# Kernel tuning notes

Measured on AMD Instinct MI355X. Metric: run time of the kernel, lower is better.

The kernel has to match this reference:

```python
import jax, jax.numpy as jnp
import numpy as np

TAU = 1.0
LOSS_WEIGHT = 1.0
N = 4_000_000


def setup_inputs() -> dict:
    key = jax.random.key(0)
    k1, k2 = jax.random.split(key)

    def make_boxes(k):
        u = jax.random.uniform(k, (N, 5), dtype=jnp.float32)
        xy = u[:, :2] * 1024.0                 # centers in a 1024px image
        wh = u[:, 2:4] * 100.0 + 4.0           # box sizes in [4, 104)
        r = (u[:, 4:5] - 0.5) * jnp.pi         # angle in [-pi/2, pi/2)
        return jnp.concatenate([xy, wh, r], axis=-1)

    return {"pred": make_boxes(k1), "target": make_boxes(k2)}


def xy_wh_r_2_xy_sigma(xywhr):
    """(N,5) rbox -> (mu (N,2), sigma (N,2,2)) via R @ (S/2)^2 @ R^T closed form."""
    xy = xywhr[..., :2]
    wh = jnp.clip(xywhr[..., 2:4], 1e-7, 1e7)
    r = xywhr[..., 4]
    c, s = jnp.cos(r), jnp.sin(r)
    a = (0.5 * wh[..., 0]) ** 2  # (w/2)^2
    b = (0.5 * wh[..., 1]) ** 2  # (h/2)^2
    s00 = a * c * c + b * s * s
    s11 = a * s * s + b * c * c
    s01 = (a - b) * s * c
    sigma = jnp.stack(
        [jnp.stack([s00, s01], -1), jnp.stack([s01, s11], -1)], -2
    )  # (N,2,2)
    return xy, sigma


def _det2(m):
    return m[..., 0, 0] * m[..., 1, 1] - m[..., 0, 1] * m[..., 1, 0]


def _inv2(m):
    det = _det2(m)
    adj = jnp.stack(
        [jnp.stack([m[..., 1, 1], -m[..., 0, 1]], -1),
         jnp.stack([-m[..., 1, 0], m[..., 0, 0]], -1)], -2)
    return adj / det[..., None, None]


def kld_loss(mu_p, sigma_p, mu_t, sigma_t, tau):
    delta = mu_p - mu_t                                # (N,2)
    sigma_t_inv = _inv2(sigma_t)                       # (N,2,2)
    # delta^T Sigma_t^{-1} delta
    term1 = jnp.einsum('ni,nij,nj->n', delta, sigma_t_inv, delta)
    # tr(Sigma_t^{-1} Sigma_p) + log(det Sigma_t / det Sigma_p)
    tr = jnp.einsum('nij,nji->n', sigma_t_inv, sigma_p)
    term2 = tr + jnp.log(_det2(sigma_t) / _det2(sigma_p))
    dis = term1 + term2 - 2.0
    kl_dis = jnp.maximum(dis, 1e-6)
    # fun == 'log1p'
    loss = 1.0 - 1.0 / (tau + jnp.log1p(kl_dis))
    return loss[:, None]                               # (N,1) like torch version


def reference(pred, target):
    mu_p, sigma_p = xy_wh_r_2_xy_sigma(pred)
    mu_t, sigma_t = xy_wh_r_2_xy_sigma(target)
    return kld_loss(mu_p, sigma_p, mu_t, sigma_t, TAU) * LOSS_WEIGHT
```

## Files before the change

kernel.cpp:

```cpp
#include <hip/hip_runtime.h>
#include <math.h>

#define TAU_CONST 1.0f
#define BLOCK 256

#define INV_PI 0.31830988618f
#define LN2    0.69314718056f

__device__ __forceinline__ float fast_rcp(float x) { return __builtin_amdgcn_rcpf(x); }
__device__ __forceinline__ float fast_log2(float x) { return __builtin_amdgcn_logf(x); }

__device__ __forceinline__ float kld_row(const float* p, const float* t) {
    float pw = fminf(fmaxf(p[2], 1e-7f), 1e7f), ph = fminf(fmaxf(p[3], 1e-7f), 1e7f);
    float tw = fminf(fmaxf(t[2], 1e-7f), 1e7f), th = fminf(fmaxf(t[3], 1e-7f), 1e7f);
    float ap = 0.25f * pw * pw, bp = 0.25f * ph * ph;
    float at = 0.25f * tw * tw, bt = 0.25f * th * th;

    float revp = p[4] * INV_PI;
    float revt = t[4] * INV_PI;
    float s2p = __builtin_amdgcn_sinf(revp), c2p = __builtin_amdgcn_cosf(revp);
    float s2t = __builtin_amdgcn_sinf(revt), c2t = __builtin_amdgcn_cosf(revt);

    float hp = 0.5f * (ap + bp), qp = 0.5f * (ap - bp);
    float ht = 0.5f * (at + bt), qt = 0.5f * (at - bt);
    float p00 = hp + qp * c2p, p11 = hp - qp * c2p, p01 = qp * s2p;
    float t00 = ht + qt * c2t, t11 = ht - qt * c2t, t01 = qt * s2t;

    float dp = ap * bp;
    float dt = at * bt;
    float inv_dt = fast_rcp(dt);

    float dx = p[0] - t[0], dy = p[1] - t[1];
    float term1 = (dx * dx * t11 - 2.0f * dx * dy * t01 + dy * dy * t00) * inv_dt;
    float tr    = (t11 * p00 + t00 * p11 - 2.0f * t01 * p01) * inv_dt;
    float logterm = LN2 * fast_log2(dt * fast_rcp(dp));

    float dis = term1 + tr + logterm - 2.0f;
    float kl  = fmaxf(dis, 1e-6f);
    float denom = TAU_CONST + LN2 * fast_log2(1.0f + kl);
    return 1.0f - fast_rcp(denom);
}

__global__ void __launch_bounds__(BLOCK) gdloss_hw_kernel(const float4* __restrict__ pred4,
                                                          const float4* __restrict__ targ4,
                                                          float4* __restrict__ out4, int n4) {
    int tid = blockIdx.x * blockDim.x + threadIdx.x;
    if (tid >= n4) return;
    float4 pv[5], tv[5];
    const long b = 5L * tid;
#pragma unroll
    for (int k = 0; k < 5; ++k) {
        pv[k] = pred4[b + k];
        tv[k] = targ4[b + k];
    }
    const float* P = (const float*)pv;
    const float* T = (const float*)tv;
    float4 o;
    o.x = kld_row(P + 0,  T + 0);
    o.y = kld_row(P + 5,  T + 5);
    o.z = kld_row(P + 10, T + 10);
    o.w = kld_row(P + 15, T + 15);
    out4[tid] = o;
}

__global__ void gdloss_tail_kernel(const float* __restrict__ pred,
                                   const float* __restrict__ target,
                                   float* __restrict__ out, int start, int n) {
    int i = start + blockIdx.x * blockDim.x + threadIdx.x;
    if (i >= n) return;
    float p[5], t[5];
#pragma unroll
    for (int k = 0; k < 5; ++k) { p[k] = pred[5 * i + k]; t[k] = target[5 * i + k]; }
    out[i] = kld_row(p, t);
}

extern "C" void kernel_launch(void* const* d_in, const int* in_sizes, int n_in,
                              void* d_out, int out_size, void* d_ws, size_t ws_size,
                              hipStream_t stream) {
    const float* pred   = (const float*)d_in[0];
    const float* target = (const float*)d_in[1];
    float* out = (float*)d_out;
    const int n = in_sizes[0] / 5;
    const int n4 = n / 4;
    if (n4 > 0) {
        int blocks = (n4 + BLOCK - 1) / BLOCK;
        gdloss_hw_kernel<<<blocks, BLOCK, 0, stream>>>((const float4*)pred,
                                                       (const float4*)target,
                                                       (float4*)out, n4);
    }
    if (n - n4 * 4 > 0) {
        gdloss_tail_kernel<<<1, 64, 0, stream>>>(pred, target, out, n4 * 4, n);
    }
}
```

Baseline: 178.4 us.

## Stage input tiles into LDS via async global_load_lds with double buffering

Replaces the one-row-group-per-thread kernel with a persistent grid-stride kernel. Each wavefront copies 256-row tiles of pred and target straight into LDS using global_load_lds and double-buffers them, so the next tile's loads overlap the current tile's math. The aim is to hide memory latency and make the input reads fully coalesced. In exchange it adds LDS traffic, a hand-written vmcnt wait, and a capped grid of 1024 blocks of 128 threads, which may lower occupancy.

```diff
diff --git a/kernel.cpp b/kernel.cpp
--- a/kernel.cpp
+++ b/kernel.cpp
@@ -2,10 +2,15 @@
 #include <math.h>
 
 #define TAU_CONST 1.0f
-#define BLOCK 256
+#define BLOCK 128
+#define WPB (BLOCK / 64)
+#define NBLOCKS 1024
+#define ROWS_PER_TILE 256
 
 #define INV_PI 0.31830988618f
 #define LN2    0.69314718056f
+
+typedef float vfloat4 __attribute__((ext_vector_type(4)));
 
 __device__ __forceinline__ float fast_rcp(float x) { return __builtin_amdgcn_rcpf(x); }
 __device__ __forceinline__ float fast_log2(float x) { return __builtin_amdgcn_logf(x); }
@@ -15,52 +20,72 @@
     float tw = fminf(fmaxf(t[2], 1e-7f), 1e7f), th = fminf(fmaxf(t[3], 1e-7f), 1e7f);
     float ap = 0.25f * pw * pw, bp = 0.25f * ph * ph;
     float at = 0.25f * tw * tw, bt = 0.25f * th * th;
-
-    float revp = p[4] * INV_PI;
-    float revt = t[4] * INV_PI;
-    float s2p = __builtin_amdgcn_sinf(revp), c2p = __builtin_amdgcn_cosf(revp);
-    float s2t = __builtin_amdgcn_sinf(revt), c2t = __builtin_amdgcn_cosf(revt);
-
+    float s2p = __builtin_amdgcn_sinf(p[4] * INV_PI), c2p = __builtin_amdgcn_cosf(p[4] * INV_PI);
+    float s2t = __builtin_amdgcn_sinf(t[4] * INV_PI), c2t = __builtin_amdgcn_cosf(t[4] * INV_PI);
     float hp = 0.5f * (ap + bp), qp = 0.5f * (ap - bp);
     float ht = 0.5f * (at + bt), qt = 0.5f * (at - bt);
     float p00 = hp + qp * c2p, p11 = hp - qp * c2p, p01 = qp * s2p;
     float t00 = ht + qt * c2t, t11 = ht - qt * c2t, t01 = qt * s2t;
-
-    float dp = ap * bp;
-    float dt = at * bt;
+    float dp = ap * bp, dt = at * bt;
     float inv_dt = fast_rcp(dt);
-
     float dx = p[0] - t[0], dy = p[1] - t[1];
     float term1 = (dx * dx * t11 - 2.0f * dx * dy * t01 + dy * dy * t00) * inv_dt;
     float tr    = (t11 * p00 + t00 * p11 - 2.0f * t01 * p01) * inv_dt;
     float logterm = LN2 * fast_log2(dt * fast_rcp(dp));
-
     float dis = term1 + tr + logterm - 2.0f;
     float kl  = fmaxf(dis, 1e-6f);
-    float denom = TAU_CONST + LN2 * fast_log2(1.0f + kl);
-    return 1.0f - fast_rcp(denom);
+    return 1.0f - fast_rcp(TAU_CONST + LN2 * fast_log2(1.0f + kl));
 }
 
-__global__ void __launch_bounds__(BLOCK) gdloss_hw_kernel(const float4* __restrict__ pred4,
-                                                          const float4* __restrict__ targ4,
-                                                          float4* __restrict__ out4, int n4) {
-    int tid = blockIdx.x * blockDim.x + threadIdx.x;
-    if (tid >= n4) return;
-    float4 pv[5], tv[5];
-    const long b = 5L * tid;
+__device__ __forceinline__ void stage_tile(const char* predB, const char* targB,
+                                           int t, float* buf, int lane) {
+    const char* gp = predB + (size_t)t * 5120 + (size_t)lane * 16;
+    const char* gt = targB + (size_t)t * 5120 + (size_t)lane * 16;
+    float* lp = buf;
+    float* lt = buf + 1280;
 #pragma unroll
-    for (int k = 0; k < 5; ++k) {
-        pv[k] = pred4[b + k];
-        tv[k] = targ4[b + k];
+    for (int i = 0; i < 5; ++i) {
+        __builtin_amdgcn_global_load_lds((const __attribute__((address_space(1))) void*)(gp + i * 1024),
+                                         (__attribute__((address_space(3))) void*)(lp + i * 256), 16, 0, 0);
+        __builtin_amdgcn_global_load_lds((const __attribute__((address_space(1))) void*)(gt + i * 1024),
+                                         (__attribute__((address_space(3))) void*)(lt + i * 256), 16, 0, 0);
     }
-    const float* P = (const float*)pv;
-    const float* T = (const float*)tv;
-    float4 o;
-    o.x = kld_row(P + 0,  T + 0);
-    o.y = kld_row(P + 5,  T + 5);
-    o.z = kld_row(P + 10, T + 10);
-    o.w = kld_row(P + 15, T + 15);
-    out4[tid] = o;
+}
+
+__global__ void __launch_bounds__(BLOCK) gdloss_ldsdma_kernel(const char* __restrict__ predB,
+                                                              const char* __restrict__ targB,
+                                                              vfloat4* __restrict__ out4,
+                                                              int ntiles) {
+    __shared__ __align__(16) float sbuf[WPB][2][2560];
+    const int lane = threadIdx.x & 63;
+    const int w    = threadIdx.x >> 6;
+    const int gw   = blockIdx.x * WPB + w;
+    const int stride = gridDim.x * WPB;
+
+    int t = gw;
+    if (t >= ntiles) return;
+    stage_tile(predB, targB, t, &sbuf[w][0][0], lane);
+    int cur = 0;
+    while (true) {
+        const int tn = t + stride;
+        const bool more = (tn < ntiles);
+        if (more) {
+            stage_tile(predB, targB, tn, &sbuf[w][cur ^ 1][0], lane);
+            asm volatile("s_waitcnt vmcnt(10)" ::: "memory");
+        } else {
+            asm volatile("s_waitcnt vmcnt(0)" ::: "memory");
+        }
+        const float* P = &sbuf[w][cur][0]    + lane * 20;
+        const float* T = &sbuf[w][cur][1280] + lane * 20;
+        vfloat4 o;
+        o.x = kld_row(P + 0,  T + 0);
+        o.y = kld_row(P + 5,  T + 5);
+        o.z = kld_row(P + 10, T + 10);
+        o.w = kld_row(P + 15, T + 15);
+        out4[(size_t)t * 64 + lane] = o;
+        if (!more) break;
+        t = tn; cur ^= 1;
+    }
 }
 
 __global__ void gdloss_tail_kernel(const float* __restrict__ pred,
@@ -81,14 +106,17 @@
     const float* target = (const float*)d_in[1];
     float* out = (float*)d_out;
     const int n = in_sizes[0] / 5;
-    const int n4 = n / 4;
-    if (n4 > 0) {
-        int blocks = (n4 + BLOCK - 1) / BLOCK;
-        gdloss_hw_kernel<<<blocks, BLOCK, 0, stream>>>((const float4*)pred,
-                                                       (const float4*)target,
-                                                       (float4*)out, n4);
+    const int ntiles = n / ROWS_PER_TILE;
+    if (ntiles > 0) {
+        int blocks = (ntiles + WPB - 1) / WPB;
+        if (blocks > NBLOCKS) blocks = NBLOCKS;
+        gdloss_ldsdma_kernel<<<blocks, BLOCK, 0, stream>>>((const char*)pred,
+                                                           (const char*)target,
+                                                           (vfloat4*)out, ntiles);
     }
-    if (n - n4 * 4 > 0) {
-        gdloss_tail_kernel<<<1, 64, 0, stream>>>(pred, target, out, n4 * 4, n);
+    const int done = ntiles * ROWS_PER_TILE;
+    if (n - done > 0) {
+        int rem = n - done;
+        gdloss_tail_kernel<<<(rem + 255) / 256, 256, 0, stream>>>(pred, target, out, done, n);
     }
 }
```

Result: no change. 180.9 us (+1.4%).
